# Performance work log

Measured on AMD Instinct MI355X. Metric: run time of the kernel, lower is better.

The kernel has to match this reference:

```python
import jax, jax.numpy as jnp
import numpy as np

N, HIDDEN, D = 4096, 512, 64  # num_stocks, hidden_dim, graph_dim//num_heads
NEG_SLOPE = 0.2


def setup_inputs() -> dict:
    key = jax.random.key(0)
    k1, k2, k3 = jax.random.split(key, 3)
    x = jax.random.normal(k1, (N, HIDDEN), dtype=jnp.float32)
    # fc_transform.weight: Linear(hidden, D, bias=False); stored transposed for x @ W
    W = jax.random.normal(k2, (HIDDEN, D), dtype=jnp.float32) * 0.05
    # fc_attention.weight: Linear(2*D, 1, bias=False) -> vector of length 2*D
    a = jax.random.normal(k3, (2 * D,), dtype=jnp.float32) * 0.05
    return {"x": x, "W": W, "a": a}


def reference(x, W, a):
    # x: (N, hidden) -> transformed features xt: (N, D)
    xt = x @ W
    # The original materializes an (N, N, 2D) tensor of concat([x_i, x_j]) and
    # applies fc_attention. Since fc_attention is linear,
    # a^T [x_i || x_j] = a1 . x_i + a2 . x_j, so we compute scores by broadcast
    # without the N^2 * 2D intermediate.
    a1, a2 = a[:D], a[D:]
    s1 = xt @ a1  # (N,) contribution from row index i
    s2 = xt @ a2  # (N,) contribution from col index j
    e = jax.nn.leaky_relu(s1[:, None] + s2[None, :], NEG_SLOPE)  # (N, N)
    attn = jax.nn.softmax(e, axis=-1)  # softmax over neighbors j
    out = attn @ xt  # einsum 'nm,md->nd'
    return out
```

## Files before the change

kernel.cpp:

```cpp
#include <hip/hip_runtime.h>

#define NN 4096
#define HID 512
#define DD 64
#define SLOPE 0.2f
#define CH 1024
#define CL 4

__global__ __launch_bounds__(256) void k1_xt(
    const float* __restrict__ x, const float* __restrict__ W,
    const float* __restrict__ a,
    float* __restrict__ xt, float* __restrict__ s1, float* __restrict__ s2) {
  __shared__ float Wl[256 * DD];
  int tid = threadIdx.x;
  int w = tid >> 6, l = tid & 63;
  int i0 = blockIdx.x * 16 + w * 4;
  const float4* xr0 = (const float4*)(x + (size_t)(i0 + 0) * HID);
  const float4* xr1 = (const float4*)(x + (size_t)(i0 + 1) * HID);
  const float4* xr2 = (const float4*)(x + (size_t)(i0 + 2) * HID);
  const float4* xr3 = (const float4*)(x + (size_t)(i0 + 3) * HID);
  float acc0 = 0.f, acc1 = 0.f, acc2 = 0.f, acc3 = 0.f;
#pragma unroll
  for (int half = 0; half < 2; ++half) {
    __syncthreads();
    const float4* W4 = (const float4*)(W + half * 256 * DD);
    float4* Wl4 = (float4*)Wl;
#pragma unroll
    for (int u = 0; u < (256 * DD / 4) / 256; ++u)
      Wl4[u * 256 + tid] = W4[u * 256 + tid];
    __syncthreads();
#pragma unroll 2
    for (int k4 = 0; k4 < 64; ++k4) {
      int kg = half * 64 + k4;
      float4 xv0 = xr0[kg], xv1 = xr1[kg], xv2 = xr2[kg], xv3 = xr3[kg];
      int k = k4 * 4;
      float w0 = Wl[(k + 0) * DD + l];
      float w1 = Wl[(k + 1) * DD + l];
      float w2 = Wl[(k + 2) * DD + l];
      float w3 = Wl[(k + 3) * DD + l];
      acc0 = fmaf(xv0.x, w0, acc0); acc0 = fmaf(xv0.y, w1, acc0);
      acc0 = fmaf(xv0.z, w2, acc0); acc0 = fmaf(xv0.w, w3, acc0);
      acc1 = fmaf(xv1.x, w0, acc1); acc1 = fmaf(xv1.y, w1, acc1);
      acc1 = fmaf(xv1.z, w2, acc1); acc1 = fmaf(xv1.w, w3, acc1);
      acc2 = fmaf(xv2.x, w0, acc2); acc2 = fmaf(xv2.y, w1, acc2);
      acc2 = fmaf(xv2.z, w2, acc2); acc2 = fmaf(xv2.w, w3, acc2);
      acc3 = fmaf(xv3.x, w0, acc3); acc3 = fmaf(xv3.y, w1, acc3);
      acc3 = fmaf(xv3.z, w2, acc3); acc3 = fmaf(xv3.w, w3, acc3);
    }
  }
  xt[(i0 + 0) * DD + l] = acc0;
  xt[(i0 + 1) * DD + l] = acc1;
  xt[(i0 + 2) * DD + l] = acc2;
  xt[(i0 + 3) * DD + l] = acc3;
  float a1 = a[l], a2 = a[DD + l];
  float p10 = acc0 * a1, p20 = acc0 * a2;
  float p11 = acc1 * a1, p21 = acc1 * a2;
  float p12 = acc2 * a1, p22 = acc2 * a2;
  float p13 = acc3 * a1, p23 = acc3 * a2;
#pragma unroll
  for (int off = 32; off >= 1; off >>= 1) {
    p10 += __shfl_xor(p10, off, 64); p20 += __shfl_xor(p20, off, 64);
    p11 += __shfl_xor(p11, off, 64); p21 += __shfl_xor(p21, off, 64);
    p12 += __shfl_xor(p12, off, 64); p22 += __shfl_xor(p22, off, 64);
    p13 += __shfl_xor(p13, off, 64); p23 += __shfl_xor(p23, off, 64);
  }
  if (l == 0) {
    s1[i0 + 0] = p10; s2[i0 + 0] = p20;
    s1[i0 + 1] = p11; s2[i0 + 1] = p21;
    s1[i0 + 2] = p12; s2[i0 + 2] = p22;
    s1[i0 + 3] = p13; s2[i0 + 3] = p23;
  }
}

__global__ __launch_bounds__(256) void k2_rank(
    const float* __restrict__ s2, float* __restrict__ s2s, int* __restrict__ perm) {
  __shared__ float keys[NN];
  __shared__ int pc[16][17];
  int tid = threadIdx.x, b = blockIdx.x;
  const float4* s4 = (const float4*)s2;
  float4* kk = (float4*)keys;
#pragma unroll
  for (int u = 0; u < NN / 4 / 256; ++u)
    kk[u * 256 + tid] = s4[u * 256 + tid];
  __syncthreads();
  int el = tid & 15, rep = tid >> 4;
  int e = b * 16 + el;
  float ke = keys[e];
  const float4* k4p = (const float4*)keys;
  int cnt = 0;
#pragma unroll 4
  for (int q4 = rep * 64; q4 < rep * 64 + 64; ++q4) {
    float4 kv = k4p[q4];
    int q = q4 * 4;
    cnt += (kv.x < ke || (kv.x == ke && q + 0 < e)) ? 1 : 0;
    cnt += (kv.y < ke || (kv.y == ke && q + 1 < e)) ? 1 : 0;
    cnt += (kv.z < ke || (kv.z == ke && q + 2 < e)) ? 1 : 0;
    cnt += (kv.w < ke || (kv.w == ke && q + 3 < e)) ? 1 : 0;
  }
  pc[rep][el] = cnt;
  __syncthreads();
  if (tid < 16) {
    int rank = 0;
#pragma unroll
    for (int r = 0; r < 16; ++r) rank += pc[r][tid];
    s2s[rank] = keys[b * 16 + tid];
    perm[rank] = b * 16 + tid;
  }
}

__global__ __launch_bounds__(256) void k3_scan(
    const float* __restrict__ xt, const float* __restrict__ s2s,
    const int* __restrict__ perm,
    float* __restrict__ SP, float* __restrict__ SN,
    float* __restrict__ zP, float* __restrict__ zN) {
  int tid = threadIdx.x, w = tid >> 6, l = tid & 63;
  int cw = blockIdx.x * 4 + w, r0 = cw * CL;
  float evP[CL], evN[CL], xv[CL];
  int pmv[CL];
#pragma unroll
  for (int q = 0; q < CL; ++q) {
    float sv = s2s[r0 + q];
    evP[q] = expf(sv);
    evN[q] = expf(SLOPE * sv);
  }
#pragma unroll
  for (int q = 0; q < CL; ++q) pmv[q] = perm[r0 + q] * DD;
#pragma unroll
  for (int q = 0; q < CL; ++q) xv[q] = xt[pmv[q] + l];
  float aP = 0.f, aN = 0.f, azP = 0.f, azN = 0.f;
#pragma unroll
  for (int q = 0; q < CL; ++q) {
    aP = fmaf(evP[q], xv[q], aP);
    aN = fmaf(evN[q], xv[q], aN);
    azP += evP[q]; azN += evN[q];
    SP[(r0 + q) * DD + l] = aP;
    SN[(r0 + q) * DD + l] = aN;
    if (l == 0) { zP[r0 + q] = azP; zN[r0 + q] = azN; }
  }
}

__global__ __launch_bounds__(256) void k4_off(
    const float* __restrict__ SP, const float* __restrict__ SN,
    const float* __restrict__ zP, const float* __restrict__ zN,
    float* __restrict__ offP, float* __restrict__ offN,
    float* __restrict__ offZP, float* __restrict__ offZN) {
  int tid = threadIdx.x, w = tid >> 6, l = tid & 63;
  int gw = blockIdx.x * 4 + w;
  const float* src = nullptr; float* dst = nullptr; int col = 0, stride = 0;
  if (gw < 64)        { src = SP; dst = offP;  col = gw;      stride = DD; }
  else if (gw < 128)  { src = SN; dst = offN;  col = gw - 64; stride = DD; }
  else if (gw == 128) { src = zP; dst = offZP; col = 0;       stride = 1;  }
  else if (gw == 129) { src = zN; dst = offZN; col = 0;       stride = 1;  }
  if (src) {
    int c0 = 16 * l;
    float v[16], p[16];
#pragma unroll
    for (int j = 0; j < 16; ++j)
      v[j] = src[((c0 + j) * CL + CL - 1) * stride + col];
    float run = 0.f;
#pragma unroll
    for (int j = 0; j < 16; ++j) { p[j] = run; run += v[j]; }
    float T = run;
    float incl = T;
#pragma unroll
    for (int off = 1; off < 64; off <<= 1) {
      float t2 = __shfl_up(incl, off, 64);
      if (l >= off) incl += t2;
    }
    float excl = incl - T;
#pragma unroll
    for (int j = 0; j < 16; ++j)
      dst[(c0 + j) * stride + col] = excl + p[j];
    if (l == 63) dst[CH * stride + col] = incl;
  }
}

__global__ __launch_bounds__(256) void k5_out(
    const float* __restrict__ s1, const float* __restrict__ s2s,
    const float* __restrict__ SP, const float* __restrict__ SN,
    const float* __restrict__ zP, const float* __restrict__ zN,
    const float* __restrict__ offP, const float* __restrict__ offN,
    const float* __restrict__ offZP, const float* __restrict__ offZN,
    float* __restrict__ out) {
  __shared__ float keys[NN];
  int tid = threadIdx.x, w = tid >> 6, l = tid & 63, b = blockIdx.x;
  const float4* s4 = (const float4*)s2s;
  float4* kk = (float4*)keys;
#pragma unroll
  for (int u = 0; u < NN / 4 / 256; ++u)
    kk[u * 256 + tid] = s4[u * 256 + tid];
  __syncthreads();
  float totP = offP[CH * DD + l];
  float totZ = offZP[CH];
  int q0 = l & 3;
  int i = b * 16 + w * 4 + q0;
  float s1v = s1[i];
  float t = -s1v;
  int lo = 0, hi = NN;
#pragma unroll
  for (int it = 0; it < 12; ++it) {
    int mid = (lo + hi) >> 1;
    if (keys[mid] <= t) lo = mid + 1; else hi = mid;
  }
  int kq = lo;
#pragma unroll
  for (int q = 0; q < 4; ++q) {
    int kk_ = __shfl(kq, q, 64);
    float s1q = __shfl(s1v, q, 64);
    float wPq = expf(s1q);
    float wNq = expf(SLOPE * s1q);
    float FPk = 0.f, FNk = 0.f, ZPk = 0.f, ZNk = 0.f;
    if (kk_ > 0) {
      int r = kk_ - 1, c = r >> 2;
      FPk = offP[c * DD + l] + SP[r * DD + l];
      FNk = offN[c * DD + l] + SN[r * DD + l];
      ZPk = offZP[c] + zP[r];
      ZNk = offZN[c] + zN[r];
    }
    float num = wPq * (totP - FPk) + wNq * FNk;
    float den = wPq * (totZ - ZPk) + wNq * ZNk;
    out[(b * 16 + w * 4 + q) * DD + l] = num / den;
  }
}

extern "C" void kernel_launch(void* const* d_in, const int* in_sizes, int n_in,
                              void* d_out, int out_size, void* d_ws, size_t ws_size,
                              hipStream_t stream) {
  const float* x = (const float*)d_in[0];
  const float* W = (const float*)d_in[1];
  const float* a = (const float*)d_in[2];
  float* out = (float*)d_out;

  float* ws = (float*)d_ws;
  float* xt    = ws;
  float* s1    = xt + NN * DD;
  float* s2    = s1 + NN;
  float* s2s   = s2 + NN;
  int*   perm  = (int*)(s2s + NN);
  float* SP    = (float*)(perm + NN);
  float* SN    = SP + NN * DD;
  float* zP    = SN + NN * DD;
  float* zN    = zP + NN;
  float* offP  = zN + NN;
  float* offN  = offP + (CH + 1) * DD;
  float* offZP = offN + (CH + 1) * DD;
  float* offZN = offZP + (CH + 1);

  k1_xt<<<NN / 16, 256, 0, stream>>>(x, W, a, xt, s1, s2);
  k2_rank<<<NN / 16, 256, 0, stream>>>(s2, s2s, perm);
  k3_scan<<<CH / 4, 256, 0, stream>>>(xt, s2s, perm, SP, SN, zP, zN);
  k4_off<<<33, 256, 0, stream>>>(SP, SN, zP, zN, offP, offN, offZP, offZN);
  k5_out<<<NN / 16, 256, 0, stream>>>(s1, s2s, SP, SN, zP, zN,
                                      offP, offN, offZP, offZN, out);
}
```

Measured before the change: 46.74 us.

## Replace prefix-scan kernels with hierarchical block/segment/chunk sums and fused rank count

Removes the separate scan and offset kernels and the per-row prefix arrays. A single kernel now writes per-chunk, per-segment and per-block partial sums. The output kernel rebuilds each prefix by adding up to 7+7+7+8 partial terms. The binary search for the split index moves into the rank kernel as a second counting pass. This cuts the launch count from five to four and shrinks intermediate traffic, but the sums kernel runs on only 8 blocks and the output kernel does more gather work per row.

```diff
diff --git a/kernel.cpp b/kernel.cpp
--- a/kernel.cpp
+++ b/kernel.cpp
@@ -4,10 +4,11 @@
 #define HID 512
 #define DD 64
 #define SLOPE 0.2f
-#define CH 1024
-#define CL 4
-
-__global__ __launch_bounds__(256) void k1_xt(
+#define NCHUNK 512
+#define NSEG 64
+#define NBLK8 8
+
+__global__ __launch_bounds__(256) void kA_xt(
     const float* __restrict__ x, const float* __restrict__ W,
     const float* __restrict__ a,
     float* __restrict__ xt, float* __restrict__ s1, float* __restrict__ s2) {
@@ -72,10 +73,12 @@
   }
 }
 
-__global__ __launch_bounds__(256) void k2_rank(
-    const float* __restrict__ s2, float* __restrict__ s2s, int* __restrict__ perm) {
+__global__ __launch_bounds__(256) void kB_rank(
+    const float* __restrict__ s2, const float* __restrict__ s1,
+    float* __restrict__ s2s, int* __restrict__ perm, int* __restrict__ kidx) {
   __shared__ float keys[NN];
   __shared__ int pc[16][17];
+  __shared__ int pk[16][17];
   int tid = threadIdx.x, b = blockIdx.x;
   const float4* s4 = (const float4*)s2;
   float4* kk = (float4*)keys;
@@ -86,8 +89,9 @@
   int el = tid & 15, rep = tid >> 4;
   int e = b * 16 + el;
   float ke = keys[e];
+  float te = -s1[e];
   const float4* k4p = (const float4*)keys;
-  int cnt = 0;
+  int cnt = 0, ck = 0;
 #pragma unroll 4
   for (int q4 = rep * 64; q4 < rep * 64 + 64; ++q4) {
     float4 kv = k4p[q4];
@@ -96,129 +100,170 @@
     cnt += (kv.y < ke || (kv.y == ke && q + 1 < e)) ? 1 : 0;
     cnt += (kv.z < ke || (kv.z == ke && q + 2 < e)) ? 1 : 0;
     cnt += (kv.w < ke || (kv.w == ke && q + 3 < e)) ? 1 : 0;
+    ck += (kv.x <= te) ? 1 : 0;
+    ck += (kv.y <= te) ? 1 : 0;
+    ck += (kv.z <= te) ? 1 : 0;
+    ck += (kv.w <= te) ? 1 : 0;
   }
   pc[rep][el] = cnt;
+  pk[rep][el] = ck;
   __syncthreads();
   if (tid < 16) {
-    int rank = 0;
-#pragma unroll
-    for (int r = 0; r < 16; ++r) rank += pc[r][tid];
+    int rank = 0, kx = 0;
+#pragma unroll
+    for (int r = 0; r < 16; ++r) { rank += pc[r][tid]; kx += pk[r][tid]; }
     s2s[rank] = keys[b * 16 + tid];
     perm[rank] = b * 16 + tid;
-  }
-}
-
-__global__ __launch_bounds__(256) void k3_scan(
+    kidx[b * 16 + tid] = kx;
+  }
+}
+
+__global__ __launch_bounds__(512) void kC_sums(
     const float* __restrict__ xt, const float* __restrict__ s2s,
     const int* __restrict__ perm,
-    float* __restrict__ SP, float* __restrict__ SN,
-    float* __restrict__ zP, float* __restrict__ zN) {
-  int tid = threadIdx.x, w = tid >> 6, l = tid & 63;
-  int cw = blockIdx.x * 4 + w, r0 = cw * CL;
-  float evP[CL], evN[CL], xv[CL];
-  int pmv[CL];
-#pragma unroll
-  for (int q = 0; q < CL; ++q) {
-    float sv = s2s[r0 + q];
-    evP[q] = expf(sv);
-    evN[q] = expf(SLOPE * sv);
-  }
-#pragma unroll
-  for (int q = 0; q < CL; ++q) pmv[q] = perm[r0 + q] * DD;
-#pragma unroll
-  for (int q = 0; q < CL; ++q) xv[q] = xt[pmv[q] + l];
-  float aP = 0.f, aN = 0.f, azP = 0.f, azN = 0.f;
-#pragma unroll
-  for (int q = 0; q < CL; ++q) {
-    aP = fmaf(evP[q], xv[q], aP);
-    aN = fmaf(evN[q], xv[q], aN);
-    azP += evP[q]; azN += evN[q];
-    SP[(r0 + q) * DD + l] = aP;
-    SN[(r0 + q) * DD + l] = aN;
-    if (l == 0) { zP[r0 + q] = azP; zN[r0 + q] = azN; }
-  }
-}
-
-__global__ __launch_bounds__(256) void k4_off(
-    const float* __restrict__ SP, const float* __restrict__ SN,
-    const float* __restrict__ zP, const float* __restrict__ zN,
-    float* __restrict__ offP, float* __restrict__ offN,
-    float* __restrict__ offZP, float* __restrict__ offZN) {
-  int tid = threadIdx.x, w = tid >> 6, l = tid & 63;
-  int gw = blockIdx.x * 4 + w;
-  const float* src = nullptr; float* dst = nullptr; int col = 0, stride = 0;
-  if (gw < 64)        { src = SP; dst = offP;  col = gw;      stride = DD; }
-  else if (gw < 128)  { src = SN; dst = offN;  col = gw - 64; stride = DD; }
-  else if (gw == 128) { src = zP; dst = offZP; col = 0;       stride = 1;  }
-  else if (gw == 129) { src = zN; dst = offZN; col = 0;       stride = 1;  }
-  if (src) {
-    int c0 = 16 * l;
-    float v[16], p[16];
-#pragma unroll
-    for (int j = 0; j < 16; ++j)
-      v[j] = src[((c0 + j) * CL + CL - 1) * stride + col];
-    float run = 0.f;
-#pragma unroll
-    for (int j = 0; j < 16; ++j) { p[j] = run; run += v[j]; }
-    float T = run;
-    float incl = T;
-#pragma unroll
-    for (int off = 1; off < 64; off <<= 1) {
-      float t2 = __shfl_up(incl, off, 64);
-      if (l >= off) incl += t2;
+    float2* __restrict__ EPN,
+    float* __restrict__ CSP, float* __restrict__ CSN, float2* __restrict__ CZ,
+    float* __restrict__ SGP, float* __restrict__ SGN, float2* __restrict__ SZ,
+    float* __restrict__ BSP, float* __restrict__ BSN, float2* __restrict__ BZ) {
+  __shared__ float2 evL[512];
+  __shared__ float segPL[8][64], segNL[8][64];
+  __shared__ float2 szL[8];
+  int tid = threadIdx.x, w = tid >> 6, l = tid & 63, B = blockIdx.x;
+  int segBase = B * 512 + w * 64;
+  int seg = B * 8 + w;
+
+  int row = segBase + l;
+  float key = s2s[row];
+  float eP = __expf(key) * 0.f + expf(key);
+  float eN = expf(SLOPE * key);
+  EPN[row] = make_float2(eP, eN);
+  evL[w * 64 + l] = make_float2(eP, eN);
+  int pmv = perm[row];
+
+  float zp = eP, zn = eN;
+#pragma unroll
+  for (int off = 1; off <= 4; off <<= 1) {
+    zp += __shfl_xor(zp, off, 64);
+    zn += __shfl_xor(zn, off, 64);
+  }
+  if ((l & 7) == 0) CZ[seg * 8 + (l >> 3)] = make_float2(zp, zn);
+#pragma unroll
+  for (int off = 8; off <= 32; off <<= 1) {
+    zp += __shfl_xor(zp, off, 64);
+    zn += __shfl_xor(zn, off, 64);
+  }
+  if (l == 0) { SZ[seg] = make_float2(zp, zn); szL[w] = make_float2(zp, zn); }
+
+  float segP = 0.f, segN = 0.f;
+#pragma unroll
+  for (int c = 0; c < 8; ++c) {
+    float cP = 0.f, cN = 0.f;
+#pragma unroll
+    for (int rr = 0; rr < 8; ++rr) {
+      int pm = __shfl(pmv, c * 8 + rr, 64);
+      float xv = xt[pm * DD + l];
+      float2 ev = evL[w * 64 + c * 8 + rr];
+      cP = fmaf(ev.x, xv, cP);
+      cN = fmaf(ev.y, xv, cN);
     }
-    float excl = incl - T;
-#pragma unroll
-    for (int j = 0; j < 16; ++j)
-      dst[(c0 + j) * stride + col] = excl + p[j];
-    if (l == 63) dst[CH * stride + col] = incl;
-  }
-}
-
-__global__ __launch_bounds__(256) void k5_out(
-    const float* __restrict__ s1, const float* __restrict__ s2s,
-    const float* __restrict__ SP, const float* __restrict__ SN,
-    const float* __restrict__ zP, const float* __restrict__ zN,
-    const float* __restrict__ offP, const float* __restrict__ offN,
-    const float* __restrict__ offZP, const float* __restrict__ offZN,
+    CSP[(seg * 8 + c) * DD + l] = cP;
+    CSN[(seg * 8 + c) * DD + l] = cN;
+    segP += cP; segN += cN;
+  }
+  SGP[seg * DD + l] = segP;
+  SGN[seg * DD + l] = segN;
+  segPL[w][l] = segP; segNL[w][l] = segN;
+  __syncthreads();
+
+  if (w == 0) {
+    float bP = 0.f, bN = 0.f;
+#pragma unroll
+    for (int s = 0; s < 8; ++s) { bP += segPL[s][l]; bN += segNL[s][l]; }
+    BSP[B * DD + l] = bP;
+    BSN[B * DD + l] = bN;
+    if (l == 0) {
+      float2 bz = make_float2(0.f, 0.f);
+#pragma unroll
+      for (int s = 0; s < 8; ++s) { bz.x += szL[s].x; bz.y += szL[s].y; }
+      BZ[B] = bz;
+    }
+  }
+}
+
+__global__ __launch_bounds__(256) void kD_out(
+    const float* __restrict__ xt, const float* __restrict__ s1,
+    const int* __restrict__ perm, const int* __restrict__ kidx,
+    const float2* __restrict__ EPN,
+    const float* __restrict__ CSP, const float* __restrict__ CSN,
+    const float2* __restrict__ CZ,
+    const float* __restrict__ SGP, const float* __restrict__ SGN,
+    const float2* __restrict__ SZ,
+    const float* __restrict__ BSP, const float* __restrict__ BSN,
+    const float2* __restrict__ BZ,
     float* __restrict__ out) {
-  __shared__ float keys[NN];
   int tid = threadIdx.x, w = tid >> 6, l = tid & 63, b = blockIdx.x;
-  const float4* s4 = (const float4*)s2s;
-  float4* kk = (float4*)keys;
-#pragma unroll
-  for (int u = 0; u < NN / 4 / 256; ++u)
-    kk[u * 256 + tid] = s4[u * 256 + tid];
-  __syncthreads();
-  float totP = offP[CH * DD + l];
-  float totZ = offZP[CH];
-  int q0 = l & 3;
-  int i = b * 16 + w * 4 + q0;
+  int i = b * 16 + w * 4 + (l & 3);
   float s1v = s1[i];
-  float t = -s1v;
-  int lo = 0, hi = NN;
-#pragma unroll
-  for (int it = 0; it < 12; ++it) {
-    int mid = (lo + hi) >> 1;
-    if (keys[mid] <= t) lo = mid + 1; else hi = mid;
-  }
-  int kq = lo;
+  int kq = kidx[i];
+
+  float totP = 0.f, totZ = 0.f;
+#pragma unroll
+  for (int j = 0; j < 8; ++j) {
+    totP += BSP[j * DD + l];
+    totZ += BZ[j].x;
+  }
+
 #pragma unroll
   for (int q = 0; q < 4; ++q) {
     int kk_ = __shfl(kq, q, 64);
     float s1q = __shfl(s1v, q, 64);
-    float wPq = expf(s1q);
-    float wNq = expf(SLOPE * s1q);
+    float wP = expf(s1q);
+    float wN = expf(SLOPE * s1q);
     float FPk = 0.f, FNk = 0.f, ZPk = 0.f, ZNk = 0.f;
     if (kk_ > 0) {
-      int r = kk_ - 1, c = r >> 2;
-      FPk = offP[c * DD + l] + SP[r * DD + l];
-      FNk = offN[c * DD + l] + SN[r * DD + l];
-      ZPk = offZP[c] + zP[r];
-      ZNk = offZN[c] + zN[r];
+      int r = kk_ - 1;
+      int br = r >> 9, sr = (r >> 6) & 7, cr = (r >> 3) & 7;
+      int segg = r >> 6, base = r & ~7, rlim = r & 7;
+#pragma unroll
+      for (int j = 0; j < 7; ++j) {
+        float vP = BSP[j * DD + l], vN = BSN[j * DD + l];
+        float2 z = BZ[j];
+        bool p = j < br;
+        FPk += p ? vP : 0.f; FNk += p ? vN : 0.f;
+        ZPk += p ? z.x : 0.f; ZNk += p ? z.y : 0.f;
+      }
+#pragma unroll
+      for (int j = 0; j < 7; ++j) {
+        int idx = (br << 3) + j;
+        float vP = SGP[idx * DD + l], vN = SGN[idx * DD + l];
+        float2 z = SZ[idx];
+        bool p = j < sr;
+        FPk += p ? vP : 0.f; FNk += p ? vN : 0.f;
+        ZPk += p ? z.x : 0.f; ZNk += p ? z.y : 0.f;
+      }
+#pragma unroll
+      for (int j = 0; j < 7; ++j) {
+        int idx = (segg << 3) + j;
+        float vP = CSP[idx * DD + l], vN = CSN[idx * DD + l];
+        float2 z = CZ[idx];
+        bool p = j < cr;
+        FPk += p ? vP : 0.f; FNk += p ? vN : 0.f;
+        ZPk += p ? z.x : 0.f; ZNk += p ? z.y : 0.f;
+      }
+#pragma unroll
+      for (int j = 0; j < 8; ++j) {
+        int rw = base + j;
+        float2 ev = EPN[rw];
+        int pm = perm[rw];
+        float xv = xt[pm * DD + l];
+        bool p = j <= rlim;
+        FPk = fmaf(p ? ev.x : 0.f, xv, FPk);
+        FNk = fmaf(p ? ev.y : 0.f, xv, FNk);
+        ZPk += p ? ev.x : 0.f; ZNk += p ? ev.y : 0.f;
+      }
     }
-    float num = wPq * (totP - FPk) + wNq * FNk;
-    float den = wPq * (totZ - ZPk) + wNq * ZNk;
+    float num = wP * (totP - FPk) + wN * FNk;
+    float den = wP * (totZ - ZPk) + wN * ZNk;
     out[(b * 16 + w * 4 + q) * DD + l] = num / den;
   }
 }
@@ -232,24 +277,27 @@
   float* out = (float*)d_out;
 
   float* ws = (float*)d_ws;
-  float* xt    = ws;
-  float* s1    = xt + NN * DD;
-  float* s2    = s1 + NN;
-  float* s2s   = s2 + NN;
-  int*   perm  = (int*)(s2s + NN);
-  float* SP    = (float*)(perm + NN);
-  float* SN    = SP + NN * DD;
-  float* zP    = SN + NN * DD;
-  float* zN    = zP + NN;
-  float* offP  = zN + NN;
-  float* offN  = offP + (CH + 1) * DD;
-  float* offZP = offN + (CH + 1) * DD;
-  float* offZN = offZP + (CH + 1);
-
-  k1_xt<<<NN / 16, 256, 0, stream>>>(x, W, a, xt, s1, s2);
-  k2_rank<<<NN / 16, 256, 0, stream>>>(s2, s2s, perm);
-  k3_scan<<<CH / 4, 256, 0, stream>>>(xt, s2s, perm, SP, SN, zP, zN);
-  k4_off<<<33, 256, 0, stream>>>(SP, SN, zP, zN, offP, offN, offZP, offZN);
-  k5_out<<<NN / 16, 256, 0, stream>>>(s1, s2s, SP, SN, zP, zN,
-                                      offP, offN, offZP, offZN, out);
-}
+  float*  xt   = ws;
+  float*  s1   = xt + NN * DD;
+  float*  s2   = s1 + NN;
+  float*  s2s  = s2 + NN;
+  int*    perm = (int*)(s2s + NN);
+  int*    kidx = perm + NN;
+  float2* EPN  = (float2*)(kidx + NN);
+  float*  CSP  = (float*)(EPN + NN);
+  float*  CSN  = CSP + NCHUNK * DD;
+  float2* CZ   = (float2*)(CSN + NCHUNK * DD);
+  float*  SGP  = (float*)(CZ + NCHUNK);
+  float*  SGN  = SGP + NSEG * DD;
+  float2* SZ   = (float2*)(SGN + NSEG * DD);
+  float*  BSP  = (float*)(SZ + NSEG);
+  float*  BSN  = BSP + NBLK8 * DD;
+  float2* BZ   = (float2*)(BSN + NBLK8 * DD);
+
+  kA_xt<<<NN / 16, 256, 0, stream>>>(x, W, a, xt, s1, s2);
+  kB_rank<<<NN / 16, 256, 0, stream>>>(s2, s1, s2s, perm, kidx);
+  kC_sums<<<NBLK8, 512, 0, stream>>>(xt, s2s, perm, EPN, CSP, CSN, CZ,
+                                     SGP, SGN, SZ, BSP, BSN, BZ);
+  kD_out<<<NN / 16, 256, 0, stream>>>(xt, s1, perm, kidx, EPN, CSP, CSN, CZ,
+                                      SGP, SGN, SZ, BSP, BSN, BZ, out);
+}
```

After: 46.57 us. No clear change (-0.4%).
